# Performance work log

Measured on AMD Instinct MI355X. Metric: run time of the kernel, lower is better.

The kernel has to match this reference:

```python
import jax, jax.numpy as jnp
import numpy as np

N_NODES = 40000
N_EDGES = 640000
D = 128
BN_EPS = 1e-5


def setup_inputs() -> dict:
    key = jax.random.key(0)
    k1, k2, k3, k4 = jax.random.split(key, 4)
    x = jax.random.normal(k1, (N_NODES, D), dtype=jnp.float32)
    edge_index = jax.random.randint(k2, (2, N_EDGES), 0, N_NODES, dtype=jnp.int64)
    W = jax.random.normal(k3, (D, D), dtype=jnp.float32) * (1.0 / np.sqrt(D))
    b = jax.random.normal(k4, (D,), dtype=jnp.float32) * 0.01
    gamma = jnp.ones((D,), dtype=jnp.float32)
    beta = jnp.zeros((D,), dtype=jnp.float32)
    return {"x": x, "edge_index": edge_index, "W": W, "b": b,
            "gamma": gamma, "beta": beta}


def reference(x, edge_index, W, b, gamma, beta):
    num_nodes = x.shape[0]
    # linear projection: [N, D_in] @ [D_in, D_out]
    h = x @ W.T + b
    src, dst = edge_index[0], edge_index[1]
    # gather messages from source nodes, scatter-add into destinations
    msgs = jax.ops.segment_sum(h[src], dst, num_segments=num_nodes)  # [N, D]
    # in-degree of each destination node, clamped to >= 1
    deg = jax.ops.segment_sum(jnp.ones_like(dst, dtype=h.dtype), dst,
                              num_segments=num_nodes)
    deg = jnp.maximum(deg, 1.0)
    h = h + msgs / deg[:, None]
    # BatchNorm1d (training mode: biased batch statistics over nodes)
    mean = jnp.mean(h, axis=0)
    var = jnp.mean(jnp.square(h - mean), axis=0)
    out = (h - mean) * jax.lax.rsqrt(var + BN_EPS) * gamma + beta
    return jax.nn.relu(out)
```

## Files before the change

kernel.cpp:

```cpp
#include <hip/hip_runtime.h>

#define NN 40000
#define NE 640000
#define DD 128
#define MAXDEG 64
#define BN_EPS 1e-5f
#define GEMM_BLKS 625
#define BUCKET_BLKS 128
#define CHUNKA 5000
#define EPT 20
#define NBKT 313
#define NPB 128
#define CAP 2432
#define PADK 132
#define POISON 0xAAAAAAAAu

typedef __attribute__((ext_vector_type(8))) short short8;
typedef __attribute__((ext_vector_type(4))) float f32x4;
typedef __attribute__((ext_vector_type(2))) float f32x2;

__device__ __forceinline__ unsigned int rb16(float x) {
  unsigned int u = __float_as_uint(x);
  return (u + 0x7fffu + ((u >> 16) & 1u)) >> 16;
}

__global__ __launch_bounds__(256) void fat_kernel(
    const float* __restrict__ x, const float* __restrict__ W,
    const float* __restrict__ bias, unsigned int* __restrict__ hbf,
    unsigned int* __restrict__ hfp8, const int* __restrict__ ei,
    unsigned int* __restrict__ gcur, unsigned int* __restrict__ ebkt) {
  __shared__ unsigned int smem[64 * PADK / 2];
  const int tid = threadIdx.x;

  if (blockIdx.x >= GEMM_BLKS) {
    unsigned int* cnts = smem;
    const int b = blockIdx.x - GEMM_BLKS;
    for (int i = tid; i < NBKT; i += 256) cnts[i] = 0u;
    __syncthreads();
    const int e0 = b * CHUNKA;
    unsigned pk[EPT];
#pragma unroll
    for (int j = 0; j < EPT; ++j) {
      const int i = tid + j * 256;
      if (i < CHUNKA) {
        const unsigned s = (unsigned)ei[e0 + i];
        const unsigned d = (unsigned)ei[NE + e0 + i];
        pk[j] = s | (d << 16);
        atomicAdd(&cnts[d >> 7], 1u);
      }
    }
    __syncthreads();
    for (int k = tid; k < NBKT; k += 256) {
      const unsigned c = cnts[k];
      cnts[k] = atomicAdd(&gcur[k], c) - POISON;
    }
    __syncthreads();
#pragma unroll
    for (int j = 0; j < EPT; ++j) {
      const int i = tid + j * 256;
      if (i < CHUNKA) {
        const unsigned d = pk[j] >> 16;
        const unsigned pos = atomicAdd(&cnts[d >> 7], 1u);
        if (pos < CAP) ebkt[(size_t)(d >> 7) * CAP + pos] = pk[j];
      }
    }
    return;
  }

  const int node0 = blockIdx.x * 64;
  const int wave = tid >> 6;
  const int lane = tid & 63;
  const int m = lane & 15;
  const int g = lane >> 4;
  const int row = node0 + wave * 16 + m;
  const float* xr = x + (size_t)row * DD;

  float4 xa[8];
#pragma unroll
  for (int ks = 0; ks < 4; ++ks) {
    xa[2 * ks]     = *reinterpret_cast<const float4*>(xr + ks * 32 + g * 8);
    xa[2 * ks + 1] = *reinterpret_cast<const float4*>(xr + ks * 32 + g * 8 + 4);
  }
  short8 a[4];
#pragma unroll
  for (int ks = 0; ks < 4; ++ks) {
    short8 aa;
    aa[0] = (short)rb16(xa[2 * ks].x);
    aa[1] = (short)rb16(xa[2 * ks].y);
    aa[2] = (short)rb16(xa[2 * ks].z);
    aa[3] = (short)rb16(xa[2 * ks].w);
    aa[4] = (short)rb16(xa[2 * ks + 1].x);
    aa[5] = (short)rb16(xa[2 * ks + 1].y);
    aa[6] = (short)rb16(xa[2 * ks + 1].z);
    aa[7] = (short)rb16(xa[2 * ks + 1].w);
    a[ks] = aa;
  }

  f32x4 acc[8];
#pragma unroll
  for (int ct = 0; ct < 8; ++ct) acc[ct] = (f32x4){0.f, 0.f, 0.f, 0.f};

#pragma unroll
  for (int ks = 0; ks < 4; ++ks) {
    const int ko = ks * 32 + g * 8;
#pragma unroll
    for (int ct = 0; ct < 8; ++ct) {
      const float* wr = W + (size_t)(ct * 16 + m) * DD + ko;
      const float4 w0 = *reinterpret_cast<const float4*>(wr);
      const float4 w1 = *reinterpret_cast<const float4*>(wr + 4);
      short8 bb;
      bb[0] = (short)rb16(w0.x);
      bb[1] = (short)rb16(w0.y);
      bb[2] = (short)rb16(w0.z);
      bb[3] = (short)rb16(w0.w);
      bb[4] = (short)rb16(w1.x);
      bb[5] = (short)rb16(w1.y);
      bb[6] = (short)rb16(w1.z);
      bb[7] = (short)rb16(w1.w);
      acc[ct] = __builtin_amdgcn_mfma_f32_16x16x32_bf16(a[ks], bb, acc[ct], 0, 0, 0);
    }
  }

  unsigned short* xs = (unsigned short*)smem;
#pragma unroll
  for (int ct = 0; ct < 8; ++ct) {
    const int ch = ct * 16 + m;
    const float bv = bias[ch];
#pragma unroll
    for (int reg = 0; reg < 4; ++reg) {
      const int nrow = wave * 16 + g * 4 + reg;
      xs[nrow * PADK + ch] = (unsigned short)rb16(acc[ct][reg] + bv);
    }
  }
  __syncthreads();
#pragma unroll
  for (int it = 0; it < 4; ++it) {
    const int flat = it * 256 + tid;
    const int r = flat >> 4;
    const int c8 = flat & 15;
    const int gn = node0 + r;
    const uint4 o = *reinterpret_cast<const uint4*>(&xs[r * PADK + c8 * 8]);
    *reinterpret_cast<uint4*>(hbf + (size_t)gn * 64 + c8 * 4) = o;
    const float f0 = __uint_as_float(o.x << 16);
    const float f1 = __uint_as_float(o.x & 0xffff0000u);
    const float f2 = __uint_as_float(o.y << 16);
    const float f3 = __uint_as_float(o.y & 0xffff0000u);
    const float f4 = __uint_as_float(o.z << 16);
    const float f5 = __uint_as_float(o.z & 0xffff0000u);
    const float f6 = __uint_as_float(o.w << 16);
    const float f7 = __uint_as_float(o.w & 0xffff0000u);
    int r0 = __builtin_amdgcn_cvt_pk_fp8_f32(f0, f1, 0, false);
    r0 = __builtin_amdgcn_cvt_pk_fp8_f32(f2, f3, r0, true);
    int r1 = __builtin_amdgcn_cvt_pk_fp8_f32(f4, f5, 0, false);
    r1 = __builtin_amdgcn_cvt_pk_fp8_f32(f6, f7, r1, true);
    *reinterpret_cast<uint2*>(hfp8 + (size_t)gn * 32 + c8 * 2) =
        make_uint2((unsigned)r0, (unsigned)r1);
  }
}

__global__ __launch_bounds__(256) void place_kernel(
    const unsigned int* __restrict__ ebkt, const unsigned int* __restrict__ gcur,
    unsigned short* __restrict__ esorted, unsigned int* __restrict__ deg32) {
  __shared__ unsigned int lcur[NPB];
  __shared__ unsigned short stag[NPB * MAXDEG];
  const int tid = threadIdx.x;
  const int k = blockIdx.x;
  for (int i = tid; i < NPB; i += 256) lcur[i] = 0u;
  __syncthreads();
  int total = (int)(gcur[k] - POISON);
  total = min(total, CAP);
  const unsigned int* eb = ebkt + (size_t)k * CAP;
  for (int i = tid; i < total; i += 256) {
    const unsigned pkv = eb[i];
    const unsigned ld = (pkv >> 16) & (NPB - 1);
    const unsigned pos = atomicAdd(&lcur[ld], 1u);
    if (pos < MAXDEG) stag[ld * MAXDEG + pos] = (unsigned short)(pkv & 0xffffu);
  }
  __syncthreads();
  const int node0 = k * NPB;
#pragma unroll
  for (int it = 0; it < 4; ++it) {
    const int flat = it * 256 + tid;
    const int row = flat >> 3;
    const int c = flat & 7;
    const int gn = node0 + row;
    if (gn < NN)
      *reinterpret_cast<uint4*>(esorted + (size_t)gn * MAXDEG + c * 8) =
          *reinterpret_cast<const uint4*>(&stag[row * MAXDEG + c * 8]);
  }
  if (tid < NPB / 4) {
    unsigned dv = 0;
#pragma unroll
    for (int z = 0; z < 4; ++z) dv |= min(lcur[tid * 4 + z], 255u) << (z * 8);
    deg32[(size_t)node0 / 4 + tid] = dv;
  }
}

__global__ __launch_bounds__(256) void gather_kernel(
    const unsigned int* __restrict__ hbf, const unsigned int* __restrict__ hfp8,
    const unsigned short* __restrict__ esorted,
    const unsigned char* __restrict__ deg8, float* __restrict__ v_out,
    float* __restrict__ sums) {
  const int tid = threadIdx.x;
  const int wv = tid >> 6;
  const int lane = tid & 63;
  const int q = lane >> 4;
  const int c = lane & 15;
  const int nW = gridDim.x * 4;
  const int wid = blockIdx.x * 4 + wv;
  float s8[8], q8[8];
#pragma unroll
  for (int j = 0; j < 8; ++j) { s8[j] = 0.f; q8[j] = 0.f; }

  int n = wid;
  int deg = 0, sraw = 0;
  uint4 su = make_uint4(0u, 0u, 0u, 0u);
  if (n < NN) {
    deg = (int)deg8[n];
    sraw = (int)esorted[n * MAXDEG + lane];
    su = *reinterpret_cast<const uint4*>(hbf + (size_t)n * 64 + c * 4);
  }
  while (n < NN) {
    const int n2 = n + nW;
    int deg2 = 0, sraw2 = 0;
    uint4 su2 = make_uint4(0u, 0u, 0u, 0u);
    if (n2 < NN) {
      deg2 = (int)deg8[n2];
      sraw2 = (int)esorted[n2 * MAXDEG + lane];
      su2 = *reinterpret_cast<const uint4*>(hbf + (size_t)n2 * 64 + c * 4);
    }
    const int dcl = min(deg, MAXDEG);
    float acc[8];
#pragma unroll
    for (int j = 0; j < 8; ++j) acc[j] = 0.f;
    for (int i0 = 0; i0 < dcl; i0 += 16) {
      int id[4];
      float w[4];
#pragma unroll
      for (int j = 0; j < 4; ++j) {
        const int e = i0 + q + 4 * j;
        const int idv = __shfl(sraw, min(e, MAXDEG - 1), 64);
        const bool vld = e < dcl;
        id[j] = vld ? idv : n;
        w[j] = vld ? 1.f : 0.f;
      }
#pragma unroll
      for (int j = 0; j < 4; ++j) {
        const uint2 u =
            *reinterpret_cast<const uint2*>(hfp8 + (size_t)id[j] * 32 + c * 2);
        const f32x2 p01 = __builtin_amdgcn_cvt_pk_f32_fp8(u.x, false);
        const f32x2 p23 = __builtin_amdgcn_cvt_pk_f32_fp8(u.x, true);
        const f32x2 p45 = __builtin_amdgcn_cvt_pk_f32_fp8(u.y, false);
        const f32x2 p67 = __builtin_amdgcn_cvt_pk_f32_fp8(u.y, true);
        acc[0] = fmaf(p01.x, w[j], acc[0]);
        acc[1] = fmaf(p01.y, w[j], acc[1]);
        acc[2] = fmaf(p23.x, w[j], acc[2]);
        acc[3] = fmaf(p23.y, w[j], acc[3]);
        acc[4] = fmaf(p45.x, w[j], acc[4]);
        acc[5] = fmaf(p45.y, w[j], acc[5]);
        acc[6] = fmaf(p67.x, w[j], acc[6]);
        acc[7] = fmaf(p67.y, w[j], acc[7]);
      }
    }
#pragma unroll
    for (int j = 0; j < 8; ++j) {
      acc[j] += __shfl_xor(acc[j], 16, 64);
      acc[j] += __shfl_xor(acc[j], 32, 64);
    }
    if (q == 0) {
      const float rdeg = 1.0f / (float)max(deg, 1);
      float v[8];
      v[0] = __uint_as_float(su.x << 16) + acc[0] * rdeg;
      v[1] = __uint_as_float(su.x & 0xffff0000u) + acc[1] * rdeg;
      v[2] = __uint_as_float(su.y << 16) + acc[2] * rdeg;
      v[3] = __uint_as_float(su.y & 0xffff0000u) + acc[3] * rdeg;
      v[4] = __uint_as_float(su.z << 16) + acc[4] * rdeg;
      v[5] = __uint_as_float(su.z & 0xffff0000u) + acc[5] * rdeg;
      v[6] = __uint_as_float(su.w << 16) + acc[6] * rdeg;
      v[7] = __uint_as_float(su.w & 0xffff0000u) + acc[7] * rdeg;
      *reinterpret_cast<float4*>(v_out + (size_t)n * DD + c * 8) =
          make_float4(v[0], v[1], v[2], v[3]);
      *reinterpret_cast<float4*>(v_out + (size_t)n * DD + c * 8 + 4) =
          make_float4(v[4], v[5], v[6], v[7]);
#pragma unroll
      for (int j = 0; j < 8; ++j) {
        s8[j] += v[j];
        q8[j] += v[j] * v[j];
      }
    }
    n = n2;
    deg = deg2;
    sraw = sraw2;
    su = su2;
  }
  __shared__ float redS[4][128];
  __shared__ float redQ[4][128];
  if (q == 0) {
#pragma unroll
    for (int j = 0; j < 8; ++j) {
      redS[wv][c * 8 + j] = s8[j];
      redQ[wv][c * 8 + j] = q8[j];
    }
  }
  __syncthreads();
  if (tid < 128) {
    const float S = redS[0][tid] + redS[1][tid] + redS[2][tid] + redS[3][tid];
    const float Q = redQ[0][tid] + redQ[1][tid] + redQ[2][tid] + redQ[3][tid];
    const int r = blockIdx.x & 7;
    unsafeAtomicAdd(&sums[r * 256 + tid], S);
    unsafeAtomicAdd(&sums[r * 256 + 128 + tid], Q);
  }
}

__global__ __launch_bounds__(256) void normalize_kernel(
    const float* __restrict__ sums, const float* __restrict__ gamma,
    const float* __restrict__ beta, float* __restrict__ out) {
  __shared__ float sc[128];
  __shared__ float sh[128];
  const int tid = threadIdx.x;
  if (tid < 128) {
    float S = 0.f, Q = 0.f;
#pragma unroll
    for (int r = 0; r < 8; ++r) {
      S += sums[r * 256 + tid];
      Q += sums[r * 256 + 128 + tid];
    }
    const float inv_n = 1.0f / (float)NN;
    const float mean = S * inv_n;
    const float var = Q * inv_n - mean * mean;
    const float inv = rsqrtf(var + BN_EPS);
    const float g = gamma[tid] * inv;
    sc[tid] = g;
    sh[tid] = beta[tid] - mean * g;
  }
  __syncthreads();
  const long total4 = (long)NN * DD / 4;
  for (long i = blockIdx.x * 256L + tid; i < total4; i += (long)gridDim.x * 256L) {
    const int c4 = (int)(i & 31);
    const float4 v = *reinterpret_cast<const float4*>(out + i * 4);
    const float4 scv = *reinterpret_cast<const float4*>(&sc[c4 * 4]);
    const float4 shv = *reinterpret_cast<const float4*>(&sh[c4 * 4]);
    float4 o;
    o.x = fmaxf(v.x * scv.x + shv.x, 0.f);
    o.y = fmaxf(v.y * scv.y + shv.y, 0.f);
    o.z = fmaxf(v.z * scv.z + shv.z, 0.f);
    o.w = fmaxf(v.w * scv.w + shv.w, 0.f);
    *reinterpret_cast<float4*>(out + i * 4) = o;
  }
}

extern "C" void kernel_launch(void* const* d_in, const int* in_sizes, int n_in,
                              void* d_out, int out_size, void* d_ws, size_t ws_size,
                              hipStream_t stream) {
  const float* x     = (const float*)d_in[0];
  const int*   ei    = (const int*)d_in[1];
  const float* W     = (const float*)d_in[2];
  const float* b     = (const float*)d_in[3];
  const float* gamma = (const float*)d_in[4];
  const float* beta  = (const float*)d_in[5];
  float* out = (float*)d_out;

  unsigned int*   hbf     = (unsigned int*)d_ws;
  unsigned int*   hfp8    = hbf + (size_t)NN * 64;
  unsigned short* esorted = (unsigned short*)(hfp8 + (size_t)NN * 32);
  unsigned int*   ebkt    = (unsigned int*)(esorted + (size_t)NN * MAXDEG);
  unsigned int*   gcur    = ebkt + (size_t)NBKT * CAP;
  unsigned int*   deg32   = gcur + NBKT;
  float*          sums    = (float*)(deg32 + 10016);

  fat_kernel<<<GEMM_BLKS + BUCKET_BLKS, 256, 0, stream>>>(
      x, W, b, hbf, hfp8, ei, gcur, ebkt);
  place_kernel<<<NBKT, 256, 0, stream>>>(ebkt, gcur, esorted, deg32);
  gather_kernel<<<2560, 256, 0, stream>>>(hbf, hfp8, esorted,
                                          (const unsigned char*)deg32, out, sums);
  normalize_kernel<<<1280, 256, 0, stream>>>(sums, gamma, beta, out);
}
```

Before: 143.4 us.

## Split fused GEMM/bucket kernel and replace stat atomics with two-level reduction

Splits the fused GEMM+edge-bucketing kernel into separate gemm and radix kernels launched back to back. It also replaces the float atomic accumulation of BatchNorm sums with per-block partial writes, reduced by a new reduce kernel and then summed in normalize. The aim is to remove atomic contention on the stats buffers. The cost is two extra kernel launches and the loss of overlap between GEMM and bucketing work. Because the fixed-order reduction no longer depends on atomics, the sums may also become deterministic.

```diff
diff --git a/kernel.cpp b/kernel.cpp
--- a/kernel.cpp
+++ b/kernel.cpp
@@ -6,12 +6,14 @@
 #define MAXDEG 64
 #define BN_EPS 1e-5f
 #define GEMM_BLKS 625
-#define BUCKET_BLKS 128
+#define RAD_BLKS 128
 #define CHUNKA 5000
 #define EPT 20
 #define NBKT 313
 #define NPB 128
 #define CAP 2432
+#define GATH_BLKS 2560
+#define RED_BLKS 40
 #define PADK 132
 #define POISON 0xAAAAAAAAu
 
@@ -24,49 +26,12 @@
   return (u + 0x7fffu + ((u >> 16) & 1u)) >> 16;
 }
 
-__global__ __launch_bounds__(256) void fat_kernel(
+__global__ __launch_bounds__(256) void gemm_kernel(
     const float* __restrict__ x, const float* __restrict__ W,
     const float* __restrict__ bias, unsigned int* __restrict__ hbf,
-    unsigned int* __restrict__ hfp8, const int* __restrict__ ei,
-    unsigned int* __restrict__ gcur, unsigned int* __restrict__ ebkt) {
-  __shared__ unsigned int smem[64 * PADK / 2];
-  const int tid = threadIdx.x;
-
-  if (blockIdx.x >= GEMM_BLKS) {
-    unsigned int* cnts = smem;
-    const int b = blockIdx.x - GEMM_BLKS;
-    for (int i = tid; i < NBKT; i += 256) cnts[i] = 0u;
-    __syncthreads();
-    const int e0 = b * CHUNKA;
-    unsigned pk[EPT];
-#pragma unroll
-    for (int j = 0; j < EPT; ++j) {
-      const int i = tid + j * 256;
-      if (i < CHUNKA) {
-        const unsigned s = (unsigned)ei[e0 + i];
-        const unsigned d = (unsigned)ei[NE + e0 + i];
-        pk[j] = s | (d << 16);
-        atomicAdd(&cnts[d >> 7], 1u);
-      }
-    }
-    __syncthreads();
-    for (int k = tid; k < NBKT; k += 256) {
-      const unsigned c = cnts[k];
-      cnts[k] = atomicAdd(&gcur[k], c) - POISON;
-    }
-    __syncthreads();
-#pragma unroll
-    for (int j = 0; j < EPT; ++j) {
-      const int i = tid + j * 256;
-      if (i < CHUNKA) {
-        const unsigned d = pk[j] >> 16;
-        const unsigned pos = atomicAdd(&cnts[d >> 7], 1u);
-        if (pos < CAP) ebkt[(size_t)(d >> 7) * CAP + pos] = pk[j];
-      }
-    }
-    return;
-  }
-
+    unsigned int* __restrict__ hfp8) {
+  __shared__ unsigned short xs[64 * PADK];
+  const int tid = threadIdx.x;
   const int node0 = blockIdx.x * 64;
   const int wave = tid >> 6;
   const int lane = tid & 63;
@@ -99,7 +64,6 @@
   f32x4 acc[8];
 #pragma unroll
   for (int ct = 0; ct < 8; ++ct) acc[ct] = (f32x4){0.f, 0.f, 0.f, 0.f};
-
 #pragma unroll
   for (int ks = 0; ks < 4; ++ks) {
     const int ko = ks * 32 + g * 8;
@@ -121,7 +85,6 @@
     }
   }
 
-  unsigned short* xs = (unsigned short*)smem;
 #pragma unroll
   for (int ct = 0; ct < 8; ++ct) {
     const int ch = ct * 16 + m;
@@ -158,6 +121,43 @@
   }
 }
 
+__global__ __launch_bounds__(256) void radixA_kernel(
+    const int* __restrict__ ei, unsigned int* __restrict__ gcur,
+    unsigned int* __restrict__ ebkt) {
+  __shared__ unsigned int cnts[NBKT];
+  const int tid = threadIdx.x;
+  const int b = blockIdx.x;
+  for (int i = tid; i < NBKT; i += 256) cnts[i] = 0u;
+  __syncthreads();
+  const int e0 = b * CHUNKA;
+  unsigned pk[EPT];
+#pragma unroll
+  for (int j = 0; j < EPT; ++j) {
+    const int i = tid + j * 256;
+    if (i < CHUNKA) {
+      const unsigned s = (unsigned)ei[e0 + i];
+      const unsigned d = (unsigned)ei[NE + e0 + i];
+      pk[j] = s | (d << 16);
+      atomicAdd(&cnts[d >> 7], 1u);
+    }
+  }
+  __syncthreads();
+  for (int k = tid; k < NBKT; k += 256) {
+    const unsigned c = cnts[k];
+    cnts[k] = atomicAdd(&gcur[k], c) - POISON;
+  }
+  __syncthreads();
+#pragma unroll
+  for (int j = 0; j < EPT; ++j) {
+    const int i = tid + j * 256;
+    if (i < CHUNKA) {
+      const unsigned d = pk[j] >> 16;
+      const unsigned pos = atomicAdd(&cnts[d >> 7], 1u);
+      if (pos < CAP) ebkt[(size_t)(d >> 7) * CAP + pos] = pk[j];
+    }
+  }
+}
+
 __global__ __launch_bounds__(256) void place_kernel(
     const unsigned int* __restrict__ ebkt, const unsigned int* __restrict__ gcur,
     unsigned short* __restrict__ esorted, unsigned int* __restrict__ deg32) {
@@ -200,7 +200,7 @@
     const unsigned int* __restrict__ hbf, const unsigned int* __restrict__ hfp8,
     const unsigned short* __restrict__ esorted,
     const unsigned char* __restrict__ deg8, float* __restrict__ v_out,
-    float* __restrict__ sums) {
+    float* __restrict__ partial) {
   const int tid = threadIdx.x;
   const int wv = tid >> 6;
   const int lane = tid & 63;
@@ -306,32 +306,41 @@
   if (tid < 128) {
     const float S = redS[0][tid] + redS[1][tid] + redS[2][tid] + redS[3][tid];
     const float Q = redQ[0][tid] + redQ[1][tid] + redQ[2][tid] + redQ[3][tid];
-    const int r = blockIdx.x & 7;
-    unsafeAtomicAdd(&sums[r * 256 + tid], S);
-    unsafeAtomicAdd(&sums[r * 256 + 128 + tid], Q);
-  }
+    partial[(size_t)blockIdx.x * 256 + tid] = S;
+    partial[(size_t)blockIdx.x * 256 + 128 + tid] = Q;
+  }
+}
+
+__global__ __launch_bounds__(256) void reduce_kernel(
+    const float* __restrict__ partial, float* __restrict__ red2) {
+  const int g = blockIdx.x;
+  const int j = threadIdx.x;
+  float a = 0.f;
+#pragma unroll 8
+  for (int k = 0; k < 64; ++k) a += partial[(size_t)(g * 64 + k) * 256 + j];
+  red2[g * 256 + j] = a;
 }
 
 __global__ __launch_bounds__(256) void normalize_kernel(
-    const float* __restrict__ sums, const float* __restrict__ gamma,
+    const float* __restrict__ red2, const float* __restrict__ gamma,
     const float* __restrict__ beta, float* __restrict__ out) {
   __shared__ float sc[128];
   __shared__ float sh[128];
   const int tid = threadIdx.x;
   if (tid < 128) {
     float S = 0.f, Q = 0.f;
-#pragma unroll
-    for (int r = 0; r < 8; ++r) {
-      S += sums[r * 256 + tid];
-      Q += sums[r * 256 + 128 + tid];
+#pragma unroll 8
+    for (int g = 0; g < RED_BLKS; ++g) {
+      S += red2[g * 256 + tid];
+      Q += red2[g * 256 + 128 + tid];
     }
     const float inv_n = 1.0f / (float)NN;
     const float mean = S * inv_n;
     const float var = Q * inv_n - mean * mean;
     const float inv = rsqrtf(var + BN_EPS);
-    const float g = gamma[tid] * inv;
-    sc[tid] = g;
-    sh[tid] = beta[tid] - mean * g;
+    const float gm = gamma[tid] * inv;
+    sc[tid] = gm;
+    sh[tid] = beta[tid] - mean * gm;
   }
   __syncthreads();
   const long total4 = (long)NN * DD / 4;
@@ -366,12 +375,14 @@
   unsigned int*   ebkt    = (unsigned int*)(esorted + (size_t)NN * MAXDEG);
   unsigned int*   gcur    = ebkt + (size_t)NBKT * CAP;
   unsigned int*   deg32   = gcur + NBKT;
-  float*          sums    = (float*)(deg32 + 10016);
-
-  fat_kernel<<<GEMM_BLKS + BUCKET_BLKS, 256, 0, stream>>>(
-      x, W, b, hbf, hfp8, ei, gcur, ebkt);
+  float*          partial = (float*)(deg32 + 10016);
+  float*          red2    = partial + (size_t)GATH_BLKS * 256;
+
+  gemm_kernel<<<GEMM_BLKS, 256, 0, stream>>>(x, W, b, hbf, hfp8);
+  radixA_kernel<<<RAD_BLKS, 256, 0, stream>>>(ei, gcur, ebkt);
   place_kernel<<<NBKT, 256, 0, stream>>>(ebkt, gcur, esorted, deg32);
-  gather_kernel<<<2560, 256, 0, stream>>>(hbf, hfp8, esorted,
-                                          (const unsigned char*)deg32, out, sums);
-  normalize_kernel<<<1280, 256, 0, stream>>>(sums, gamma, beta, out);
-}
+  gather_kernel<<<GATH_BLKS, 256, 0, stream>>>(hbf, hfp8, esorted,
+                                               (const unsigned char*)deg32, out, partial);
+  reduce_kernel<<<RED_BLKS, 256, 0, stream>>>(partial, red2);
+  normalize_kernel<<<1280, 256, 0, stream>>>(red2, gamma, beta, out);
+}
```

After: 158.2 us. +10.3%, slower.
